# Kernel tuning notes

Measured on AMD Instinct MI355X. Metric: run time of the kernel, lower is better.

## Reference

```python
import jax, jax.numpy as jnp
import numpy as np

N, E = 20000, 160000
F, H, OUT = 256, 8, 128
L = 6            # total layers -> 5 GAT layers
LM1 = L - 1
NGN = L // 3 + 1 # 3 GraphNorms
D = F // H       # 32 per head
GN_FREQ = 3
EPS = 1e-5


def setup_inputs() -> dict:
    key = jax.random.key(0)
    ks = jax.random.split(key, 12)
    x = jax.random.normal(ks[0], (N, 1), dtype=jnp.float32)
    edge_index = jax.random.randint(ks[1], (2, E), 0, N, dtype=jnp.int32)
    W0 = jax.random.normal(ks[2], (1, F), dtype=jnp.float32) * 0.1
    b0 = jnp.zeros((F,), jnp.float32)
    gat_lin = jax.random.normal(ks[3], (LM1, F, F), dtype=jnp.float32) * (1.0 / np.sqrt(F))
    att_src = jax.random.normal(ks[4], (LM1, H, D), dtype=jnp.float32) * 0.1
    att_dst = jax.random.normal(ks[5], (LM1, H, D), dtype=jnp.float32) * 0.1
    gat_bias = jnp.zeros((LM1, F), jnp.float32)
    gn_weight = jnp.ones((NGN, F), jnp.float32)
    gn_bias = jnp.zeros((NGN, F), jnp.float32)
    gn_mean_scale = jnp.ones((NGN, F), jnp.float32)
    lin_W = jax.random.normal(ks[6], (F, OUT), dtype=jnp.float32) * (1.0 / np.sqrt(F))
    lin_b = jnp.zeros((OUT,), jnp.float32)
    return {"x": x, "W0": W0, "b0": b0, "gat_lin": gat_lin, "att_src": att_src,
            "att_dst": att_dst, "gat_bias": gat_bias, "gn_weight": gn_weight,
            "gn_bias": gn_bias, "gn_mean_scale": gn_mean_scale,
            "lin_W": lin_W, "lin_b": lin_b, "edge_index": edge_index}


def _gcn_conv(x, W, b, src, dst, n):
    h = x @ W
    deg = jax.ops.segment_sum(jnp.ones(src.shape[0], h.dtype), dst, num_segments=n)
    dinv = jnp.where(deg > 0, jax.lax.rsqrt(deg), 0.0)
    norm = dinv[src] * dinv[dst]                      # [E']
    out = jax.ops.segment_sum(h[src] * norm[:, None], dst, num_segments=n)
    return out + b


def _gat_conv(x, W, a_src, a_dst, src, dst, n):
    # PyG GATConv (concat=True, negative_slope=0.2, self-loops in src/dst)
    h = (x @ W).reshape(n, H, D)
    s = jnp.einsum('nhd,hd->nh', h, a_src)            # [N,H]
    t = jnp.einsum('nhd,hd->nh', h, a_dst)
    e = jax.nn.leaky_relu(s[src] + t[dst], 0.2)       # [E',H]
    m = jax.ops.segment_max(e, dst, num_segments=n)   # per-dst softmax
    e = jnp.exp(e - m[dst])
    denom = jax.ops.segment_sum(e, dst, num_segments=n)
    alpha = e / (denom[dst] + 1e-16)
    out = jax.ops.segment_sum(h[src] * alpha[:, :, None], dst, num_segments=n)
    return out.reshape(n, F)


def _graph_norm(x, w, b, ms):
    # PyG GraphNorm with batch=None (single graph): per-feature stats over nodes
    mean = jnp.mean(x, axis=0)
    out = x - ms * mean
    var = jnp.mean(out * out, axis=0)
    return w * out * jax.lax.rsqrt(var + EPS) + b


def reference(x, W0, b0, gat_lin, att_src, att_dst, gat_bias, gn_weight, gn_bias,
              gn_mean_scale, lin_W, lin_b, edge_index):
    n = x.shape[0]
    loops = jnp.arange(n, dtype=edge_index.dtype)
    src = jnp.concatenate([edge_index[0], loops])
    dst = jnp.concatenate([edge_index[1], loops])
    h = jax.nn.relu(_gcn_conv(x, W0, b0, src, dst, n))
    for i in range(LM1):
        if i % GN_FREQ == 0:
            g = i // GN_FREQ
            h = _graph_norm(h, gn_weight[g], gn_bias[g], gn_mean_scale[g])
        out = _gat_conv(h, gat_lin[i], att_src[i], att_dst[i], src, dst, n)
        if i % GN_FREQ == 0:
            out = out + gat_bias[i]
        h = h + jax.nn.relu(out)
    return h @ lin_W + lin_b
```

## Files before the change

kernel.cpp:

```cpp
#include <hip/hip_runtime.h>
#include <hip/hip_bf16.h>
#include <stdint.h>

typedef float f32x4 __attribute__((ext_vector_type(4)));
typedef short s16x8 __attribute__((ext_vector_type(8)));

__device__ __forceinline__ float bf2f(unsigned short u) {
    union { unsigned int i; float f; } v; v.i = ((unsigned int)u) << 16; return v.f;
}
__device__ __forceinline__ unsigned short f2bf(float f) {
    union { float f; unsigned int i; } v; v.f = f;
    unsigned int x = v.i;
    return (unsigned short)((x + 0x7fffu + ((x >> 16) & 1u)) >> 16);
}
__device__ __forceinline__ void bfp(unsigned int u, float& lo, float& hi) {
    union { unsigned int i; float f; } a, b;
    a.i = u << 16; b.i = u & 0xffff0000u;
    lo = a.f; hi = b.f;
}
__device__ __forceinline__ void gload16(const void* g, void* l) {
    __builtin_amdgcn_global_load_lds(
        (const __attribute__((address_space(1))) void*)g,
        (__attribute__((address_space(3))) void*)l, 16, 0, 0);
}

__global__ void k_prep(const int* __restrict__ ei, int E, int* __restrict__ deg,
                       int CB,
                       const float* __restrict__ gat_lin,
                       const float* __restrict__ lin_W,
                       const float* __restrict__ att_src,
                       const float* __restrict__ att_dst,
                       unsigned short* __restrict__ Wt,
                       unsigned short* __restrict__ lt) {
    int bid = blockIdx.x;
    if (bid < CB) {
        int e = bid * 256 + threadIdx.x;
        if (e < E) atomicAdd(&deg[ei[E + e]], 1);
        return;
    }
    int idx = (bid - CB) * 256 + threadIdx.x;
    const int T1 = 5 * 65536;
    const int T2 = T1 + 128 * 256;
    const int T3 = T2 + 5 * 64 * 256;
    if (idx < T1) {
        int l = idx >> 16, r = idx & 0xFFFF;
        int nrow = r >> 8, k = r & 255;
        Wt[(size_t)l * 81920 + nrow * 256 + k] =
            f2bf(gat_lin[(size_t)l * 65536 + k * 256 + nrow]);
    } else if (idx < T2) {
        int j = idx - T1;
        int nrow = j >> 8, k = j & 255;
        lt[nrow * 256 + k] = f2bf(lin_W[(size_t)k * 128 + nrow]);
    } else if (idx < T3) {
        int j = idx - T2;
        int l = j >> 14, r = j & 16383;
        int row = r >> 8, k = r & 255;
        float v = 0.f;
        if (row < 16) {
            int head = row & 7;
            const float* a = (row < 8) ? (att_src + l * 256 + head * 32)
                                       : (att_dst + l * 256 + head * 32);
            const float* wr = gat_lin + (size_t)l * 65536 + k * 256 + head * 32;
#pragma unroll
            for (int d = 0; d < 32; ++d) v += wr[d] * a[d];
        }
        Wt[(size_t)l * 81920 + (256 + row) * 256 + k] = f2bf(v);
    }
}

__global__ __launch_bounds__(256) void k_bsum(const int* __restrict__ deg,
                                              int* __restrict__ bsum, int n) {
    __shared__ int buf[256];
    int i = blockIdx.x * 256 + threadIdx.x;
    buf[threadIdx.x] = (i < n) ? deg[i] + 1 : 0;
    __syncthreads();
#pragma unroll
    for (int off = 128; off > 0; off >>= 1) {
        if ((int)threadIdx.x < off) buf[threadIdx.x] += buf[threadIdx.x + off];
        __syncthreads();
    }
    if (threadIdx.x == 0) bsum[blockIdx.x] = buf[0];
}

__global__ __launch_bounds__(256) void k_scanb(const int* __restrict__ bsum,
                                               int* __restrict__ boff, int nb) {
    __shared__ int buf[256];
    int t = threadIdx.x;
    int v = (t < nb) ? bsum[t] : 0;
    buf[t] = v;
    __syncthreads();
    for (int off = 1; off < 256; off <<= 1) {
        int add = (t >= off) ? buf[t - off] : 0;
        __syncthreads();
        buf[t] += add;
        __syncthreads();
    }
    if (t < nb) boff[t] = buf[t] - v;
}

__global__ __launch_bounds__(256) void k_emit(const int* __restrict__ deg,
                                              const int* __restrict__ boff,
                                              int* __restrict__ rowptr,
                                              int* __restrict__ wo,
                                              float* __restrict__ dinv, int n) {
    __shared__ int buf[256];
    int i = blockIdx.x * 256 + threadIdx.x;
    int v = (i < n) ? deg[i] + 1 : 0;
    buf[threadIdx.x] = v;
    __syncthreads();
    for (int off = 1; off < 256; off <<= 1) {
        int add = ((int)threadIdx.x >= off) ? buf[threadIdx.x - off] : 0;
        __syncthreads();
        buf[threadIdx.x] += add;
        __syncthreads();
    }
    if (i < n) {
        int excl = boff[blockIdx.x] + buf[threadIdx.x] - v;
        rowptr[i] = excl;
        wo[i] = excl;
        dinv[i] = rsqrtf((float)v);
        if (i == n - 1) rowptr[n] = excl + v;
    }
}

__global__ void k_fill(const int* __restrict__ ei, int E, int n,
                       int* wo, int* srcs) {
    int e = blockIdx.x * blockDim.x + threadIdx.x;
    int EP = E + n;
    if (e >= EP) return;
    int s_, d_;
    if (e < E) { s_ = ei[e]; d_ = ei[E + e]; }
    else       { s_ = d_ = e - E; }
    int pos = atomicAdd(&wo[d_], 1);
    srcs[pos] = s_;
}

__global__ __launch_bounds__(256) void k_h0f(const float* __restrict__ x,
                                             const float* __restrict__ dinv,
                                             const int* __restrict__ rowptr,
                                             const int* __restrict__ srcs,
                                             const float* __restrict__ W0,
                                             const float* __restrict__ b0,
                                             unsigned short* __restrict__ hbf,
                                             int n, int Mpad) {
    int wave = threadIdx.x >> 6, lane = threadIdx.x & 63;
    int node = blockIdx.x * 4 + wave;
    if (node >= Mpad) return;
    size_t base = (size_t)node * 256 + lane * 4;
    if (node >= n) {
        ushort4 z = {0, 0, 0, 0};
        *reinterpret_cast<ushort4*>(hbf + base) = z;
        return;
    }
    int p0 = rowptr[node], p1 = rowptr[node + 1];
    float sum = 0.f;
    for (int p = p0 + lane; p < p1; p += 64) {
        int s = srcs[p];
        sum += x[s] * dinv[s];
    }
#pragma unroll
    for (int m = 1; m < 64; m <<= 1) sum += __shfl_xor(sum, m);
    float sv = sum * dinv[node];
    float4 wv = *reinterpret_cast<const float4*>(W0 + lane * 4);
    float4 bv = *reinterpret_cast<const float4*>(b0 + lane * 4);
    ushort4 o;
    o.x = f2bf(fmaxf(sv * wv.x + bv.x, 0.f));
    o.y = f2bf(fmaxf(sv * wv.y + bv.y, 0.f));
    o.z = f2bf(fmaxf(sv * wv.z + bv.z, 0.f));
    o.w = f2bf(fmaxf(sv * wv.w + bv.w, 0.f));
    *reinterpret_cast<ushort4*>(hbf + base) = o;
}

__global__ __launch_bounds__(256) void k_gn_reduce(const unsigned short* __restrict__ hbf,
                                                   float* sums, float* sumsq, int n) {
    int f = threadIdx.x;
    float s = 0.f, q = 0.f;
    for (int r = blockIdx.x; r < n; r += gridDim.x) {
        float v = bf2f(hbf[(size_t)r * 256 + f]);
        s += v; q += v * v;
    }
    atomicAdd(&sums[f], s);
    atomicAdd(&sumsq[f], q);
}

__global__ __launch_bounds__(256) void k_gnfold(const float* __restrict__ st,
                                                const float* __restrict__ w,
                                                const float* __restrict__ b,
                                                const float* __restrict__ ms,
                                                unsigned short* __restrict__ Wt,
                                                float* __restrict__ so,
                                                float* __restrict__ rowbias,
                                                float ninv) {
    __shared__ float red[256];
    int col = blockIdx.x, k = threadIdx.x;
    float mean = st[k] * ninv;
    float m2   = st[256 + k] * ninv;
    float msf  = ms[k];
    float var  = m2 + msf * mean * mean * (msf - 2.0f);
    float sc = w[k] * rsqrtf(var + 1e-5f);
    float of = b[k] - msf * mean * sc;
    size_t idx = (size_t)col * 256 + k;
    float wv = bf2f(Wt[idx]);
    red[k] = of * wv;
    __syncthreads();
#pragma unroll
    for (int off = 128; off > 0; off >>= 1) {
        if (k < off) red[k] += red[k + off];
        __syncthreads();
    }
    if (k == 0) rowbias[col] = red[0];
    Wt[idx] = f2bf(sc * wv);
    if (col == 0) { so[k] = sc; so[256 + k] = of; }
}

#define BM 64
__global__ __launch_bounds__(512) void k_gemm_mfma(
    const unsigned short* __restrict__ A,
    const unsigned short* __restrict__ Bt,
    unsigned short* __restrict__ Cb,
    float* __restrict__ Cf,
    float* __restrict__ sbuf,
    float* __restrict__ tbuf,
    const float* __restrict__ bias,
    const float* __restrict__ rowbias,
    int M, int ldc)
{
    __shared__ unsigned short As[64 * 256];
    __shared__ unsigned short Bs[64 * 256];
    const int tid = threadIdx.x;
    const int bm = blockIdx.x * BM;
    const int bn = blockIdx.y * 64;
    {
        const char* ga = (const char*)(A + (size_t)bm * 256);
        const char* gb = (const char*)(Bt + (size_t)bn * 256);
        char* la = (char*)As;
        char* lb = (char*)Bs;
#pragma unroll
        for (int i = 0; i < 4; ++i) {
            int o  = (i * 512 + tid) * 16;
            int so = o ^ (((o >> 9) & 7) << 4);
            gload16(ga + so, la + o);
            gload16(gb + so, lb + o);
        }
    }
    __syncthreads();

    const int lane = tid & 63;
    const int w  = tid >> 6;
    const int wm = (w >> 1) * 16;
    const int wn = (w & 1) * 32;
    const int r  = lane & 15, kb = lane >> 4;
    const int r4 = (lane >> 4) * 4, cc = lane & 15;
    const char* la = (const char*)As;
    const char* lb = (const char*)Bs;

    f32x4 acc[2] = {};
#pragma unroll
    for (int ks = 0; ks < 8; ++ks) {
        int row = wm + r;
        int c16 = (ks * 4 + kb) ^ (row & 7);
        s16x8 af = *(const s16x8*)(la + row * 512 + c16 * 16);
#pragma unroll
        for (int j = 0; j < 2; ++j) {
            int col = wn + j * 16 + r;
            int d16 = (ks * 4 + kb) ^ (col & 7);
            s16x8 bfr = *(const s16x8*)(lb + col * 512 + d16 * 16);
            acc[j] = __builtin_amdgcn_mfma_f32_16x16x32_bf16(af, bfr, acc[j], 0, 0, 0);
        }
    }
#pragma unroll
    for (int j = 0; j < 2; ++j) {
        int col = bn + wn + j * 16 + cc;
        float rb = rowbias ? rowbias[col] : 0.f;
#pragma unroll
        for (int q = 0; q < 4; ++q) {
            int row = bm + wm + r4 + q;
            float v = acc[j][q] + rb;
            if (Cb) {
                if (col < 256) {
                    Cb[(size_t)row * 256 + col] = f2bf(v);
                } else if (col < 264) {
                    sbuf[(size_t)row * 8 + (col - 256)] = v;
                } else if (col < 272) {
                    tbuf[(size_t)row * 8 + (col - 264)] = v;
                }
            } else if (row < M) {
                Cf[(size_t)row * ldc + col] = v + bias[col];
            }
        }
    }
}

__global__ __launch_bounds__(256) void k_fagg(const unsigned short* __restrict__ h1,
                                              const float* __restrict__ sbuf,
                                              const float* __restrict__ tbuf,
                                              const int* __restrict__ rowptr,
                                              const int* __restrict__ srcs,
                                              unsigned short* __restrict__ hbf,
                                              const float* __restrict__ bias,
                                              const float* __restrict__ so, int n) {
    int wave = threadIdx.x >> 6, lane = threadIdx.x & 63;
    int node = blockIdx.x * 4 + wave;
    if (node >= n) return;
    int p0 = rowptr[node], p1 = rowptr[node + 1];
    int hid = lane >> 5;
    int l5 = lane & 31;
    int fl = l5 * 8;
    int head = l5 >> 2;
    float tv = tbuf[node * 8 + head];
    float m = -1e30f, den = 0.f;
    float a0 = 0.f, a1 = 0.f, a2 = 0.f, a3 = 0.f;
    float a4 = 0.f, a5 = 0.f, a6 = 0.f, a7 = 0.f;
    int q = p0 + hid;
    for (; q + 2 < p1; q += 4) {
        int s0 = srcs[q], s1 = srcs[q + 2];
        float e0 = sbuf[s0 * 8 + head] + tv;
        float e1 = sbuf[s1 * 8 + head] + tv;
        uint4 v0 = *reinterpret_cast<const uint4*>(h1 + (size_t)s0 * 256 + fl);
        uint4 v1 = *reinterpret_cast<const uint4*>(h1 + (size_t)s1 * 256 + fl);
        e0 = (e0 > 0.f) ? e0 : 0.2f * e0;
        e1 = (e1 > 0.f) ? e1 : 0.2f * e1;
        float em = fmaxf(e0, e1);
        if (em > m + 8.f) {
            float sc = __expf(m - em);
            den *= sc;
            a0 *= sc; a1 *= sc; a2 *= sc; a3 *= sc;
            a4 *= sc; a5 *= sc; a6 *= sc; a7 *= sc;
            m = em;
        }
        float w0 = __expf(e0 - m), w1 = __expf(e1 - m);
        den += w0 + w1;
        float f0l, f0h, f1l, f1h;
        bfp(v0.x, f0l, f0h); bfp(v1.x, f1l, f1h);
        a0 += w0 * f0l + w1 * f1l;
        a1 += w0 * f0h + w1 * f1h;
        bfp(v0.y, f0l, f0h); bfp(v1.y, f1l, f1h);
        a2 += w0 * f0l + w1 * f1l;
        a3 += w0 * f0h + w1 * f1h;
        bfp(v0.z, f0l, f0h); bfp(v1.z, f1l, f1h);
        a4 += w0 * f0l + w1 * f1l;
        a5 += w0 * f0h + w1 * f1h;
        bfp(v0.w, f0l, f0h); bfp(v1.w, f1l, f1h);
        a6 += w0 * f0l + w1 * f1l;
        a7 += w0 * f0h + w1 * f1h;
    }
    for (; q < p1; q += 2) {
        int s0 = srcs[q];
        float e0 = sbuf[s0 * 8 + head] + tv;
        uint4 v0 = *reinterpret_cast<const uint4*>(h1 + (size_t)s0 * 256 + fl);
        e0 = (e0 > 0.f) ? e0 : 0.2f * e0;
        if (e0 > m + 8.f) {
            float sc = __expf(m - e0);
            den *= sc;
            a0 *= sc; a1 *= sc; a2 *= sc; a3 *= sc;
            a4 *= sc; a5 *= sc; a6 *= sc; a7 *= sc;
            m = e0;
        }
        float w0 = __expf(e0 - m);
        den += w0;
        float f0l, f0h;
        bfp(v0.x, f0l, f0h); a0 += w0 * f0l; a1 += w0 * f0h;
        bfp(v0.y, f0l, f0h); a2 += w0 * f0l; a3 += w0 * f0h;
        bfp(v0.z, f0l, f0h); a4 += w0 * f0l; a5 += w0 * f0h;
        bfp(v0.w, f0l, f0h); a6 += w0 * f0l; a7 += w0 * f0h;
    }
    float mo = __shfl_xor(m, 32);
    float mm = fmaxf(m, mo);
    float sc = __expf(m - mm);
    den *= sc; den += __shfl_xor(den, 32);
    a0 *= sc; a0 += __shfl_xor(a0, 32);
    a1 *= sc; a1 += __shfl_xor(a1, 32);
    a2 *= sc; a2 += __shfl_xor(a2, 32);
    a3 *= sc; a3 += __shfl_xor(a3, 32);
    a4 *= sc; a4 += __shfl_xor(a4, 32);
    a5 *= sc; a5 += __shfl_xor(a5, 32);
    a6 *= sc; a6 += __shfl_xor(a6, 32);
    a7 *= sc; a7 += __shfl_xor(a7, 32);
    if (hid) return;
    float inv = 1.0f / (den + 1e-16f);
    a0 *= inv; a1 *= inv; a2 *= inv; a3 *= inv;
    a4 *= inv; a5 *= inv; a6 *= inv; a7 *= inv;
    float b_[8] = {0.f, 0.f, 0.f, 0.f, 0.f, 0.f, 0.f, 0.f};
    if (bias) {
        float4 blo = *reinterpret_cast<const float4*>(bias + fl);
        float4 bhi = *reinterpret_cast<const float4*>(bias + fl + 4);
        b_[0] = blo.x; b_[1] = blo.y; b_[2] = blo.z; b_[3] = blo.w;
        b_[4] = bhi.x; b_[5] = bhi.y; b_[6] = bhi.z; b_[7] = bhi.w;
    }
    size_t base = (size_t)node * 256 + fl;
    uint4 hv = *reinterpret_cast<const uint4*>(hbf + base);
    float h_[8];
    bfp(hv.x, h_[0], h_[1]); bfp(hv.y, h_[2], h_[3]);
    bfp(hv.z, h_[4], h_[5]); bfp(hv.w, h_[6], h_[7]);
    if (so) {
        float4 s0v = *reinterpret_cast<const float4*>(so + fl);
        float4 s1v = *reinterpret_cast<const float4*>(so + fl + 4);
        float4 o0v = *reinterpret_cast<const float4*>(so + 256 + fl);
        float4 o1v = *reinterpret_cast<const float4*>(so + 256 + fl + 4);
        h_[0] = h_[0] * s0v.x + o0v.x; h_[1] = h_[1] * s0v.y + o0v.y;
        h_[2] = h_[2] * s0v.z + o0v.z; h_[3] = h_[3] * s0v.w + o0v.w;
        h_[4] = h_[4] * s1v.x + o1v.x; h_[5] = h_[5] * s1v.y + o1v.y;
        h_[6] = h_[6] * s1v.z + o1v.z; h_[7] = h_[7] * s1v.w + o1v.w;
    }
    float r0 = h_[0] + fmaxf(a0 + b_[0], 0.f);
    float r1 = h_[1] + fmaxf(a1 + b_[1], 0.f);
    float r2 = h_[2] + fmaxf(a2 + b_[2], 0.f);
    float r3 = h_[3] + fmaxf(a3 + b_[3], 0.f);
    float r4 = h_[4] + fmaxf(a4 + b_[4], 0.f);
    float r5 = h_[5] + fmaxf(a5 + b_[5], 0.f);
    float r6 = h_[6] + fmaxf(a6 + b_[6], 0.f);
    float r7 = h_[7] + fmaxf(a7 + b_[7], 0.f);
    uint4 o;
    o.x = (unsigned int)f2bf(r0) | ((unsigned int)f2bf(r1) << 16);
    o.y = (unsigned int)f2bf(r2) | ((unsigned int)f2bf(r3) << 16);
    o.z = (unsigned int)f2bf(r4) | ((unsigned int)f2bf(r5) << 16);
    o.w = (unsigned int)f2bf(r6) | ((unsigned int)f2bf(r7) << 16);
    *reinterpret_cast<uint4*>(hbf + base) = o;
}

extern "C" void kernel_launch(void* const* d_in, const int* in_sizes, int n_in,
                              void* d_out, int out_size, void* d_ws, size_t ws_size,
                              hipStream_t stream) {
    const float* x        = (const float*)d_in[0];
    const float* W0       = (const float*)d_in[1];
    const float* b0       = (const float*)d_in[2];
    const float* gat_lin  = (const float*)d_in[3];
    const float* att_src  = (const float*)d_in[4];
    const float* att_dst  = (const float*)d_in[5];
    const float* gat_bias = (const float*)d_in[6];
    const float* gn_w     = (const float*)d_in[7];
    const float* gn_b     = (const float*)d_in[8];
    const float* gn_ms    = (const float*)d_in[9];
    const float* lin_W    = (const float*)d_in[10];
    const float* lin_b    = (const float*)d_in[11];
    const int*   ei       = (const int*)d_in[12];

    const int n  = in_sizes[0];
    const int E  = in_sizes[12] / 2;
    const int EP = E + n;
    const int Mpad = ((n + BM - 1) / BM) * BM;
    const int nb = (n + 255) / 256;

    char* w = (char*)d_ws;
    unsigned short* hbf = (unsigned short*)w; w += (size_t)Mpad * 256 * 2;
    unsigned short* h1  = (unsigned short*)w; w += (size_t)Mpad * 256 * 2;
    float* sbuf = (float*)w;                  w += (size_t)Mpad * 8 * 4;
    float* tbuf = (float*)w;                  w += (size_t)Mpad * 8 * 4;
    unsigned short* Wt = (unsigned short*)w;  w += (size_t)5 * 320 * 256 * 2;
    unsigned short* lt = (unsigned short*)w;  w += (size_t)128 * 256 * 2;
    float* scaleoff = (float*)w;              w += 1024 * 4;
    float* rowbias  = (float*)w;              w += 640 * 4;
    float* gnstat = (float*)w;                w += 1024 * 4;
    int* deg    = (int*)w;                    w += (size_t)n * 4;
    float* dinv = (float*)w;                  w += (size_t)n * 4;
    int* rowptr = (int*)w;                    w += ((size_t)(n + 1) * 4 + 15) / 16 * 16;
    int* wo     = (int*)w;                    w += (size_t)n * 4;
    int* bsum   = (int*)w;                    w += ((size_t)nb * 4 + 15) / 16 * 16;
    int* boff   = (int*)w;                    w += ((size_t)nb * 4 + 15) / 16 * 16;
    int* srcs   = (int*)w;                    w += (size_t)EP * 4;

    const int B256 = 256;
    auto cdiv = [](int a, int b) { return (a + b - 1) / b; };

    hipMemsetAsync(gnstat, 0, 1024 * 4 + (size_t)n * 4, stream);

    const int CB = cdiv(E, B256);
    const int WPREP = 5 * 65536 + 128 * 256 + 5 * 64 * 256;
    k_prep<<<CB + cdiv(WPREP, B256), B256, 0, stream>>>(
        ei, E, deg, CB, gat_lin, lin_W, att_src, att_dst, Wt, lt);

    k_bsum<<<nb, 256, 0, stream>>>(deg, bsum, n);
    k_scanb<<<1, 256, 0, stream>>>(bsum, boff, nb);
    k_emit<<<nb, 256, 0, stream>>>(deg, boff, rowptr, wo, dinv, n);
    k_fill<<<cdiv(EP, B256), B256, 0, stream>>>(ei, E, n, wo, srcs);

    k_h0f<<<cdiv(Mpad, 4), 256, 0, stream>>>(x, dinv, rowptr, srcs, W0, b0, hbf, n, Mpad);

    const float ninv = 1.0f / (float)n;
    const int gx = Mpad / BM;

    for (int i = 0; i < 5; ++i) {
        const float* rb = nullptr;
        const float* so = nullptr;
        if (i % 3 == 0) {
            int g = i / 3;
            k_gn_reduce<<<256, 256, 0, stream>>>(hbf, gnstat + g * 512,
                                                 gnstat + g * 512 + 256, n);
            k_gnfold<<<320, 256, 0, stream>>>(gnstat + g * 512, gn_w + g * 256,
                                              gn_b + g * 256, gn_ms + g * 256,
                                              Wt + (size_t)i * 81920,
                                              scaleoff + g * 512, rowbias + g * 320, ninv);
            rb = rowbias + g * 320;
            so = scaleoff + g * 512;
        }
        k_gemm_mfma<<<dim3(gx, 5), 512, 0, stream>>>(
            hbf, Wt + (size_t)i * 81920, h1, nullptr, sbuf, tbuf, nullptr, rb,
            n, 256);
        k_fagg<<<cdiv(n, 4), 256, 0, stream>>>(
            h1, sbuf, tbuf, rowptr, srcs, hbf,
            (i % 3 == 0) ? gat_bias + i * 256 : nullptr, so, n);
    }

    k_gemm_mfma<<<dim3(gx, 2), 512, 0, stream>>>(
        hbf, lt, nullptr, (float*)d_out, nullptr, nullptr, lin_b, nullptr,
        n, 128);
}
```

Baseline: 282.0 us.

## Fuse whole GNN pipeline into one persistent cooperative megakernel

Replaces the chain of about twenty small kernel launches (CSR build, GCN layer, GraphNorm, GEMMs, aggregations) with a single cooperative kernel. Phases are separated by grid-wide syncs, and the GEMM becomes a persistent tile loop. The aim is to remove per-launch overhead and the idle gaps between the many short kernels. In exchange it adds grid-sync costs, runs each phase on a capped grid size, and keeps the multi-kernel path as a fallback.

```diff
diff --git a/kernel.cpp b/kernel.cpp
--- a/kernel.cpp
+++ b/kernel.cpp
@@ -1,6 +1,9 @@
 #include <hip/hip_runtime.h>
+#include <hip/hip_cooperative_groups.h>
 #include <hip/hip_bf16.h>
 #include <stdint.h>
+
+namespace cg = cooperative_groups;
 
 typedef float f32x4 __attribute__((ext_vector_type(4)));
 typedef short s16x8 __attribute__((ext_vector_type(8)));
@@ -24,284 +27,124 @@
         (__attribute__((address_space(3))) void*)l, 16, 0, 0);
 }
 
-__global__ void k_prep(const int* __restrict__ ei, int E, int* __restrict__ deg,
-                       int CB,
-                       const float* __restrict__ gat_lin,
-                       const float* __restrict__ lin_W,
-                       const float* __restrict__ att_src,
-                       const float* __restrict__ att_dst,
-                       unsigned short* __restrict__ Wt,
-                       unsigned short* __restrict__ lt) {
-    int bid = blockIdx.x;
-    if (bid < CB) {
-        int e = bid * 256 + threadIdx.x;
-        if (e < E) atomicAdd(&deg[ei[E + e]], 1);
-        return;
-    }
-    int idx = (bid - CB) * 256 + threadIdx.x;
+struct Params {
+    const float *x, *W0, *b0, *gat_lin, *att_src, *att_dst, *gat_bias;
+    const float *gn_w, *gn_b, *gn_ms, *lin_W, *lin_b;
+    const int* ei;
+    float* out;
+    unsigned short *hbf, *h1, *Wt, *lt;
+    float *sbuf, *tbuf, *scaleoff, *rowbias, *gnstat, *dinv;
+    int *deg, *rowptr, *wo, *bsum, *srcs;
+    int n, E, EP, Mpad, nb;
+};
+
+__device__ __forceinline__ void wconv_body(const Params& P, int idx) {
     const int T1 = 5 * 65536;
     const int T2 = T1 + 128 * 256;
-    const int T3 = T2 + 5 * 64 * 256;
     if (idx < T1) {
         int l = idx >> 16, r = idx & 0xFFFF;
         int nrow = r >> 8, k = r & 255;
-        Wt[(size_t)l * 81920 + nrow * 256 + k] =
-            f2bf(gat_lin[(size_t)l * 65536 + k * 256 + nrow]);
+        P.Wt[(size_t)l * 81920 + nrow * 256 + k] =
+            f2bf(P.gat_lin[(size_t)l * 65536 + k * 256 + nrow]);
     } else if (idx < T2) {
         int j = idx - T1;
         int nrow = j >> 8, k = j & 255;
-        lt[nrow * 256 + k] = f2bf(lin_W[(size_t)k * 128 + nrow]);
-    } else if (idx < T3) {
+        P.lt[nrow * 256 + k] = f2bf(P.lin_W[(size_t)k * 128 + nrow]);
+    } else {
         int j = idx - T2;
         int l = j >> 14, r = j & 16383;
         int row = r >> 8, k = r & 255;
         float v = 0.f;
         if (row < 16) {
             int head = row & 7;
-            const float* a = (row < 8) ? (att_src + l * 256 + head * 32)
-                                       : (att_dst + l * 256 + head * 32);
-            const float* wr = gat_lin + (size_t)l * 65536 + k * 256 + head * 32;
+            const float* a = (row < 8) ? (P.att_src + l * 256 + head * 32)
+                                       : (P.att_dst + l * 256 + head * 32);
+            const float* wr = P.gat_lin + (size_t)l * 65536 + k * 256 + head * 32;
 #pragma unroll
             for (int d = 0; d < 32; ++d) v += wr[d] * a[d];
         }
-        Wt[(size_t)l * 81920 + (256 + row) * 256 + k] = f2bf(v);
-    }
-}
-
-__global__ __launch_bounds__(256) void k_bsum(const int* __restrict__ deg,
-                                              int* __restrict__ bsum, int n) {
-    __shared__ int buf[256];
-    int i = blockIdx.x * 256 + threadIdx.x;
-    buf[threadIdx.x] = (i < n) ? deg[i] + 1 : 0;
-    __syncthreads();
-#pragma unroll
-    for (int off = 128; off > 0; off >>= 1) {
-        if ((int)threadIdx.x < off) buf[threadIdx.x] += buf[threadIdx.x + off];
-        __syncthreads();
-    }
-    if (threadIdx.x == 0) bsum[blockIdx.x] = buf[0];
-}
-
-__global__ __launch_bounds__(256) void k_scanb(const int* __restrict__ bsum,
-                                               int* __restrict__ boff, int nb) {
-    __shared__ int buf[256];
-    int t = threadIdx.x;
-    int v = (t < nb) ? bsum[t] : 0;
-    buf[t] = v;
-    __syncthreads();
-    for (int off = 1; off < 256; off <<= 1) {
-        int add = (t >= off) ? buf[t - off] : 0;
-        __syncthreads();
-        buf[t] += add;
-        __syncthreads();
-    }
-    if (t < nb) boff[t] = buf[t] - v;
-}
-
-__global__ __launch_bounds__(256) void k_emit(const int* __restrict__ deg,
-                                              const int* __restrict__ boff,
-                                              int* __restrict__ rowptr,
-                                              int* __restrict__ wo,
-                                              float* __restrict__ dinv, int n) {
-    __shared__ int buf[256];
-    int i = blockIdx.x * 256 + threadIdx.x;
-    int v = (i < n) ? deg[i] + 1 : 0;
-    buf[threadIdx.x] = v;
-    __syncthreads();
-    for (int off = 1; off < 256; off <<= 1) {
-        int add = ((int)threadIdx.x >= off) ? buf[threadIdx.x - off] : 0;
-        __syncthreads();
-        buf[threadIdx.x] += add;
-        __syncthreads();
-    }
-    if (i < n) {
-        int excl = boff[blockIdx.x] + buf[threadIdx.x] - v;
-        rowptr[i] = excl;
-        wo[i] = excl;
-        dinv[i] = rsqrtf((float)v);
-        if (i == n - 1) rowptr[n] = excl + v;
-    }
-}
-
-__global__ void k_fill(const int* __restrict__ ei, int E, int n,
-                       int* wo, int* srcs) {
-    int e = blockIdx.x * blockDim.x + threadIdx.x;
-    int EP = E + n;
-    if (e >= EP) return;
-    int s_, d_;
-    if (e < E) { s_ = ei[e]; d_ = ei[E + e]; }
-    else       { s_ = d_ = e - E; }
-    int pos = atomicAdd(&wo[d_], 1);
-    srcs[pos] = s_;
-}
-
-__global__ __launch_bounds__(256) void k_h0f(const float* __restrict__ x,
-                                             const float* __restrict__ dinv,
-                                             const int* __restrict__ rowptr,
-                                             const int* __restrict__ srcs,
-                                             const float* __restrict__ W0,
-                                             const float* __restrict__ b0,
-                                             unsigned short* __restrict__ hbf,
-                                             int n, int Mpad) {
-    int wave = threadIdx.x >> 6, lane = threadIdx.x & 63;
-    int node = blockIdx.x * 4 + wave;
-    if (node >= Mpad) return;
-    size_t base = (size_t)node * 256 + lane * 4;
-    if (node >= n) {
-        ushort4 z = {0, 0, 0, 0};
-        *reinterpret_cast<ushort4*>(hbf + base) = z;
-        return;
-    }
-    int p0 = rowptr[node], p1 = rowptr[node + 1];
-    float sum = 0.f;
-    for (int p = p0 + lane; p < p1; p += 64) {
-        int s = srcs[p];
-        sum += x[s] * dinv[s];
-    }
-#pragma unroll
-    for (int m = 1; m < 64; m <<= 1) sum += __shfl_xor(sum, m);
-    float sv = sum * dinv[node];
-    float4 wv = *reinterpret_cast<const float4*>(W0 + lane * 4);
-    float4 bv = *reinterpret_cast<const float4*>(b0 + lane * 4);
-    ushort4 o;
-    o.x = f2bf(fmaxf(sv * wv.x + bv.x, 0.f));
-    o.y = f2bf(fmaxf(sv * wv.y + bv.y, 0.f));
-    o.z = f2bf(fmaxf(sv * wv.z + bv.z, 0.f));
-    o.w = f2bf(fmaxf(sv * wv.w + bv.w, 0.f));
-    *reinterpret_cast<ushort4*>(hbf + base) = o;
-}
-
-__global__ __launch_bounds__(256) void k_gn_reduce(const unsigned short* __restrict__ hbf,
-                                                   float* sums, float* sumsq, int n) {
-    int f = threadIdx.x;
-    float s = 0.f, q = 0.f;
-    for (int r = blockIdx.x; r < n; r += gridDim.x) {
-        float v = bf2f(hbf[(size_t)r * 256 + f]);
-        s += v; q += v * v;
-    }
-    atomicAdd(&sums[f], s);
-    atomicAdd(&sumsq[f], q);
-}
-
-__global__ __launch_bounds__(256) void k_gnfold(const float* __restrict__ st,
-                                                const float* __restrict__ w,
-                                                const float* __restrict__ b,
-                                                const float* __restrict__ ms,
-                                                unsigned short* __restrict__ Wt,
-                                                float* __restrict__ so,
-                                                float* __restrict__ rowbias,
-                                                float ninv) {
-    __shared__ float red[256];
-    int col = blockIdx.x, k = threadIdx.x;
-    float mean = st[k] * ninv;
-    float m2   = st[256 + k] * ninv;
-    float msf  = ms[k];
-    float var  = m2 + msf * mean * mean * (msf - 2.0f);
-    float sc = w[k] * rsqrtf(var + 1e-5f);
-    float of = b[k] - msf * mean * sc;
-    size_t idx = (size_t)col * 256 + k;
-    float wv = bf2f(Wt[idx]);
-    red[k] = of * wv;
-    __syncthreads();
-#pragma unroll
-    for (int off = 128; off > 0; off >>= 1) {
-        if (k < off) red[k] += red[k + off];
-        __syncthreads();
-    }
-    if (k == 0) rowbias[col] = red[0];
-    Wt[idx] = f2bf(sc * wv);
-    if (col == 0) { so[k] = sc; so[256 + k] = of; }
-}
-
-#define BM 64
-__global__ __launch_bounds__(512) void k_gemm_mfma(
-    const unsigned short* __restrict__ A,
-    const unsigned short* __restrict__ Bt,
-    unsigned short* __restrict__ Cb,
-    float* __restrict__ Cf,
-    float* __restrict__ sbuf,
-    float* __restrict__ tbuf,
-    const float* __restrict__ bias,
-    const float* __restrict__ rowbias,
-    int M, int ldc)
+        P.Wt[(size_t)l * 81920 + (256 + row) * 256 + k] = f2bf(v);
+    }
+}
+
+__device__ __forceinline__ void gemm_phase(
+    const unsigned short* A, const unsigned short* Bt,
+    unsigned short* Cb, float* Cf, float* sbuf, float* tbuf,
+    const float* bias, const float* rowbias,
+    int M, int ldc, int npan, int Mpad,
+    unsigned short* As, unsigned short* Bs)
 {
-    __shared__ unsigned short As[64 * 256];
-    __shared__ unsigned short Bs[64 * 256];
     const int tid = threadIdx.x;
-    const int bm = blockIdx.x * BM;
-    const int bn = blockIdx.y * 64;
-    {
-        const char* ga = (const char*)(A + (size_t)bm * 256);
-        const char* gb = (const char*)(Bt + (size_t)bn * 256);
-        char* la = (char*)As;
-        char* lb = (char*)Bs;
-#pragma unroll
-        for (int i = 0; i < 4; ++i) {
-            int o  = (i * 512 + tid) * 16;
-            int so = o ^ (((o >> 9) & 7) << 4);
-            gload16(ga + so, la + o);
-            gload16(gb + so, lb + o);
-        }
-    }
-    __syncthreads();
-
+    const int gx = Mpad >> 6;
+    const int ntiles = gx * npan;
     const int lane = tid & 63;
     const int w  = tid >> 6;
     const int wm = (w >> 1) * 16;
     const int wn = (w & 1) * 32;
     const int r  = lane & 15, kb = lane >> 4;
     const int r4 = (lane >> 4) * 4, cc = lane & 15;
-    const char* la = (const char*)As;
-    const char* lb = (const char*)Bs;
-
-    f32x4 acc[2] = {};
-#pragma unroll
-    for (int ks = 0; ks < 8; ++ks) {
-        int row = wm + r;
-        int c16 = (ks * 4 + kb) ^ (row & 7);
-        s16x8 af = *(const s16x8*)(la + row * 512 + c16 * 16);
+    for (int t = blockIdx.x; t < ntiles; t += gridDim.x) {
+        int bx = t % gx, by = t / gx;
+        int bm = bx * 64, bn = by * 64;
+        __syncthreads();
+        {
+            const char* ga = (const char*)(A + (size_t)bm * 256);
+            const char* gb = (const char*)(Bt + (size_t)bn * 256);
+#pragma unroll
+            for (int i2 = 0; i2 < 4; ++i2) {
+                int o  = (i2 * 512 + tid) * 16;
+                int so = o ^ (((o >> 9) & 7) << 4);
+                gload16(ga + so, (char*)As + o);
+                gload16(gb + so, (char*)Bs + o);
+            }
+        }
+        __syncthreads();
+        f32x4 acc[2] = {};
+#pragma unroll
+        for (int ks = 0; ks < 8; ++ks) {
+            int row = wm + r;
+            int c16 = (ks * 4 + kb) ^ (row & 7);
+            s16x8 af = *(const s16x8*)((char*)As + row * 512 + c16 * 16);
+#pragma unroll
+            for (int j = 0; j < 2; ++j) {
+                int col = wn + j * 16 + r;
+                int d16 = (ks * 4 + kb) ^ (col & 7);
+                s16x8 bfr = *(const s16x8*)((char*)Bs + col * 512 + d16 * 16);
+                acc[j] = __builtin_amdgcn_mfma_f32_16x16x32_bf16(af, bfr, acc[j], 0, 0, 0);
+            }
+        }
 #pragma unroll
         for (int j = 0; j < 2; ++j) {
-            int col = wn + j * 16 + r;
-            int d16 = (ks * 4 + kb) ^ (col & 7);
-            s16x8 bfr = *(const s16x8*)(lb + col * 512 + d16 * 16);
-            acc[j] = __builtin_amdgcn_mfma_f32_16x16x32_bf16(af, bfr, acc[j], 0, 0, 0);
-        }
-    }
-#pragma unroll
-    for (int j = 0; j < 2; ++j) {
-        int col = bn + wn + j * 16 + cc;
-        float rb = rowbias ? rowbias[col] : 0.f;
-#pragma unroll
-        for (int q = 0; q < 4; ++q) {
-            int row = bm + wm + r4 + q;
-            float v = acc[j][q] + rb;
-            if (Cb) {
-                if (col < 256) {
-                    Cb[(size_t)row * 256 + col] = f2bf(v);
-                } else if (col < 264) {
-                    sbuf[(size_t)row * 8 + (col - 256)] = v;
-                } else if (col < 272) {
-                    tbuf[(size_t)row * 8 + (col - 264)] = v;
+            int col = bn + wn + j * 16 + cc;
+            float rbv = rowbias ? rowbias[col] : 0.f;
+#pragma unroll
+            for (int q2 = 0; q2 < 4; ++q2) {
+                int row = bm + wm + r4 + q2;
+                float v = acc[j][q2] + rbv;
+                if (Cb) {
+                    if (col < 256) {
+                        Cb[(size_t)row * 256 + col] = f2bf(v);
+                    } else if (col < 264) {
+                        sbuf[(size_t)row * 8 + (col - 256)] = v;
+                    } else if (col < 272) {
+                        tbuf[(size_t)row * 8 + (col - 264)] = v;
+                    }
+                } else if (row < M) {
+                    Cf[(size_t)row * ldc + col] = v + bias[col];
                 }
-            } else if (row < M) {
-                Cf[(size_t)row * ldc + col] = v + bias[col];
             }
         }
     }
 }
 
-__global__ __launch_bounds__(256) void k_fagg(const unsigned short* __restrict__ h1,
-                                              const float* __restrict__ sbuf,
-                                              const float* __restrict__ tbuf,
-                                              const int* __restrict__ rowptr,
-                                              const int* __restrict__ srcs,
-                                              unsigned short* __restrict__ hbf,
-                                              const float* __restrict__ bias,
-                                              const float* __restrict__ so, int n) {
-    int wave = threadIdx.x >> 6, lane = threadIdx.x & 63;
-    int node = blockIdx.x * 4 + wave;
-    if (node >= n) return;
+__device__ __forceinline__ void fagg_body(
+    const unsigned short* __restrict__ h1,
+    const float* __restrict__ sbuf, const float* __restrict__ tbuf,
+    const int* __restrict__ rowptr, const int* __restrict__ srcs,
+    unsigned short* __restrict__ hbf,
+    const float* __restrict__ bias, const float* __restrict__ so,
+    int node, int lane)
+{
     int p0 = rowptr[node], p1 = rowptr[node + 1];
     int hid = lane >> 5;
     int l5 = lane & 31;
@@ -418,90 +261,439 @@
     *reinterpret_cast<uint4*>(hbf + base) = o;
 }
 
-extern "C" void kernel_launch(void* const* d_in, const int* in_sizes, int n_in,
-                              void* d_out, int out_size, void* d_ws, size_t ws_size,
-                              hipStream_t stream) {
-    const float* x        = (const float*)d_in[0];
-    const float* W0       = (const float*)d_in[1];
-    const float* b0       = (const float*)d_in[2];
-    const float* gat_lin  = (const float*)d_in[3];
-    const float* att_src  = (const float*)d_in[4];
-    const float* att_dst  = (const float*)d_in[5];
-    const float* gat_bias = (const float*)d_in[6];
-    const float* gn_w     = (const float*)d_in[7];
-    const float* gn_b     = (const float*)d_in[8];
-    const float* gn_ms    = (const float*)d_in[9];
-    const float* lin_W    = (const float*)d_in[10];
-    const float* lin_b    = (const float*)d_in[11];
-    const int*   ei       = (const int*)d_in[12];
-
-    const int n  = in_sizes[0];
-    const int E  = in_sizes[12] / 2;
-    const int EP = E + n;
-    const int Mpad = ((n + BM - 1) / BM) * BM;
-    const int nb = (n + 255) / 256;
-
-    char* w = (char*)d_ws;
-    unsigned short* hbf = (unsigned short*)w; w += (size_t)Mpad * 256 * 2;
-    unsigned short* h1  = (unsigned short*)w; w += (size_t)Mpad * 256 * 2;
-    float* sbuf = (float*)w;                  w += (size_t)Mpad * 8 * 4;
-    float* tbuf = (float*)w;                  w += (size_t)Mpad * 8 * 4;
-    unsigned short* Wt = (unsigned short*)w;  w += (size_t)5 * 320 * 256 * 2;
-    unsigned short* lt = (unsigned short*)w;  w += (size_t)128 * 256 * 2;
-    float* scaleoff = (float*)w;              w += 1024 * 4;
-    float* rowbias  = (float*)w;              w += 640 * 4;
-    float* gnstat = (float*)w;                w += 1024 * 4;
-    int* deg    = (int*)w;                    w += (size_t)n * 4;
-    float* dinv = (float*)w;                  w += (size_t)n * 4;
-    int* rowptr = (int*)w;                    w += ((size_t)(n + 1) * 4 + 15) / 16 * 16;
-    int* wo     = (int*)w;                    w += (size_t)n * 4;
-    int* bsum   = (int*)w;                    w += ((size_t)nb * 4 + 15) / 16 * 16;
-    int* boff   = (int*)w;                    w += ((size_t)nb * 4 + 15) / 16 * 16;
-    int* srcs   = (int*)w;                    w += (size_t)EP * 4;
-
-    const int B256 = 256;
-    auto cdiv = [](int a, int b) { return (a + b - 1) / b; };
-
-    hipMemsetAsync(gnstat, 0, 1024 * 4 + (size_t)n * 4, stream);
-
-    const int CB = cdiv(E, B256);
-    const int WPREP = 5 * 65536 + 128 * 256 + 5 * 64 * 256;
-    k_prep<<<CB + cdiv(WPREP, B256), B256, 0, stream>>>(
-        ei, E, deg, CB, gat_lin, lin_W, att_src, att_dst, Wt, lt);
-
-    k_bsum<<<nb, 256, 0, stream>>>(deg, bsum, n);
-    k_scanb<<<1, 256, 0, stream>>>(bsum, boff, nb);
-    k_emit<<<nb, 256, 0, stream>>>(deg, boff, rowptr, wo, dinv, n);
-    k_fill<<<cdiv(EP, B256), B256, 0, stream>>>(ei, E, n, wo, srcs);
-
-    k_h0f<<<cdiv(Mpad, 4), 256, 0, stream>>>(x, dinv, rowptr, srcs, W0, b0, hbf, n, Mpad);
-
-    const float ninv = 1.0f / (float)n;
-    const int gx = Mpad / BM;
-
+__device__ __forceinline__ void h0_body(const Params& P, int node, int lane) {
+    size_t base = (size_t)node * 256 + lane * 4;
+    if (node >= P.n) {
+        ushort4 z = {0, 0, 0, 0};
+        *reinterpret_cast<ushort4*>(P.hbf + base) = z;
+        return;
+    }
+    int p0 = P.rowptr[node], p1 = P.rowptr[node + 1];
+    float sum = 0.f;
+    for (int p = p0 + lane; p < p1; p += 64) {
+        int s = P.srcs[p];
+        sum += P.x[s] * P.dinv[s];
+    }
+#pragma unroll
+    for (int m = 1; m < 64; m <<= 1) sum += __shfl_xor(sum, m);
+    float sv = sum * P.dinv[node];
+    float4 wv = *reinterpret_cast<const float4*>(P.W0 + lane * 4);
+    float4 bv = *reinterpret_cast<const float4*>(P.b0 + lane * 4);
+    ushort4 o;
+    o.x = f2bf(fmaxf(sv * wv.x + bv.x, 0.f));
+    o.y = f2bf(fmaxf(sv * wv.y + bv.y, 0.f));
+    o.z = f2bf(fmaxf(sv * wv.z + bv.z, 0.f));
+    o.w = f2bf(fmaxf(sv * wv.w + bv.w, 0.f));
+    *reinterpret_cast<ushort4*>(P.hbf + base) = o;
+}
+
+__global__ __launch_bounds__(512, 4) void k_mega(Params P) {
+    __shared__ unsigned short As[64 * 256];
+    __shared__ unsigned short Bs[64 * 256];
+    cg::grid_group grid = cg::this_grid();
+    const int tid  = threadIdx.x;
+    const int bid  = blockIdx.x;
+    const int nblk = gridDim.x;
+    const int gtid = bid * 512 + tid;
+    const int nthr = nblk * 512;
+    const int lane = tid & 63;
+    const int wid  = tid >> 6;
+    const int gw   = bid * 8 + wid;
+    const int nw   = nblk * 8;
+
+    for (int i = gtid; i < P.n; i += nthr) P.deg[i] = 0;
+    for (int i = gtid; i < 1024; i += nthr) P.gnstat[i] = 0.f;
+    {
+        const int T3 = 5 * 65536 + 128 * 256 + 5 * 64 * 256;
+        for (int idx = gtid; idx < T3; idx += nthr) wconv_body(P, idx);
+    }
+    grid.sync();
+    for (int e = gtid; e < P.E; e += nthr) atomicAdd(&P.deg[P.ei[P.E + e]], 1);
+    grid.sync();
+    for (int c = gw; c < P.nb; c += nw) {
+        int base = c * 256;
+        int s = 0;
+#pragma unroll
+        for (int j = 0; j < 4; ++j) {
+            int i = base + j * 64 + lane;
+            s += (i < P.n) ? P.deg[i] + 1 : 0;
+        }
+#pragma unroll
+        for (int m = 1; m < 64; m <<= 1) s += __shfl_xor(s, m);
+        if (lane == 0) P.bsum[c] = s;
+    }
+    grid.sync();
+    for (int c = gw; c < P.nb; c += nw) {
+        int off = 0;
+        for (int j = lane; j < c; j += 64) off += P.bsum[j];
+#pragma unroll
+        for (int m = 1; m < 64; m <<= 1) off += __shfl_xor(off, m);
+        int base = c * 256 + lane * 4;
+        int v[4];
+#pragma unroll
+        for (int j = 0; j < 4; ++j) {
+            int i = base + j;
+            v[j] = (i < P.n) ? P.deg[i] + 1 : 0;
+        }
+        int vsum = v[0] + v[1] + v[2] + v[3];
+        int incl = vsum;
+        for (int d = 1; d < 64; d <<= 1) {
+            int t = __shfl_up(incl, d);
+            if (lane >= d) incl += t;
+        }
+        int run = off + incl - vsum;
+#pragma unroll
+        for (int j = 0; j < 4; ++j) {
+            int i = base + j;
+            if (i < P.n) {
+                P.rowptr[i] = run;
+                P.wo[i] = run;
+                P.dinv[i] = rsqrtf((float)v[j]);
+                run += v[j];
+                if (i == P.n - 1) P.rowptr[P.n] = run;
+            }
+        }
+    }
+    grid.sync();
+    for (int e = gtid; e < P.EP; e += nthr) {
+        int s_, d_;
+        if (e < P.E) { s_ = P.ei[e]; d_ = P.ei[P.E + e]; }
+        else         { s_ = d_ = e - P.E; }
+        int pos = atomicAdd(&P.wo[d_], 1);
+        P.srcs[pos] = s_;
+    }
+    grid.sync();
+    for (int node = gw; node < P.Mpad; node += nw) h0_body(P, node, lane);
+    grid.sync();
     for (int i = 0; i < 5; ++i) {
         const float* rb = nullptr;
         const float* so = nullptr;
         if (i % 3 == 0) {
             int g = i / 3;
-            k_gn_reduce<<<256, 256, 0, stream>>>(hbf, gnstat + g * 512,
-                                                 gnstat + g * 512 + 256, n);
-            k_gnfold<<<320, 256, 0, stream>>>(gnstat + g * 512, gn_w + g * 256,
-                                              gn_b + g * 256, gn_ms + g * 256,
-                                              Wt + (size_t)i * 81920,
-                                              scaleoff + g * 512, rowbias + g * 320, ninv);
-            rb = rowbias + g * 320;
-            so = scaleoff + g * 512;
-        }
-        k_gemm_mfma<<<dim3(gx, 5), 512, 0, stream>>>(
-            hbf, Wt + (size_t)i * 81920, h1, nullptr, sbuf, tbuf, nullptr, rb,
-            n, 256);
-        k_fagg<<<cdiv(n, 4), 256, 0, stream>>>(
-            h1, sbuf, tbuf, rowptr, srcs, hbf,
-            (i % 3 == 0) ? gat_bias + i * 256 : nullptr, so, n);
-    }
-
-    k_gemm_mfma<<<dim3(gx, 2), 512, 0, stream>>>(
-        hbf, lt, nullptr, (float*)d_out, nullptr, nullptr, lin_b, nullptr,
-        n, 128);
-}
+            float* st = P.gnstat + g * 512;
+            {
+                int f = tid & 255, half = tid >> 8;
+                float s = 0.f, q = 0.f;
+                for (int r = bid * 2 + half; r < P.n; r += nblk * 2) {
+                    float v = bf2f(P.hbf[(size_t)r * 256 + f]);
+                    s += v; q += v * v;
+                }
+                atomicAdd(&st[f], s);
+                atomicAdd(&st[256 + f], q);
+            }
+            grid.sync();
+            {
+                unsigned short* Wl = P.Wt + (size_t)i * 81920;
+                float ninv = 1.f / (float)P.n;
+                for (int col = gw; col < 320; col += nw) {
+                    float partial = 0.f;
+#pragma unroll
+                    for (int j = 0; j < 4; ++j) {
+                        int k = lane * 4 + j;
+                        float mean = st[k] * ninv;
+                        float m2   = st[256 + k] * ninv;
+                        float msf  = P.gn_ms[g * 256 + k];
+                        float var  = m2 + msf * mean * mean * (msf - 2.0f);
+                        float sc = P.gn_w[g * 256 + k] * rsqrtf(var + 1e-5f);
+                        float of = P.gn_b[g * 256 + k] - msf * mean * sc;
+                        size_t idx = (size_t)col * 256 + k;
+                        float wv = bf2f(Wl[idx]);
+                        partial += of * wv;
+                        Wl[idx] = f2bf(sc * wv);
+                        if (col == 0) {
+                            P.scaleoff[g * 512 + k] = sc;
+                            P.scaleoff[g * 512 + 256 + k] = of;
+                        }
+                    }
+#pragma unroll
+                    for (int m = 1; m < 64; m <<= 1) partial += __shfl_xor(partial, m);
+                    if (lane == 0) P.rowbias[g * 320 + col] = partial;
+                }
+            }
+            grid.sync();
+            rb = P.rowbias + g * 320;
+            so = P.scaleoff + g * 512;
+        }
+        gemm_phase(P.hbf, P.Wt + (size_t)i * 81920, P.h1, nullptr,
+                   P.sbuf, P.tbuf, nullptr, rb, P.n, 256, 5, P.Mpad, As, Bs);
+        grid.sync();
+        {
+            const float* bias = (i % 3 == 0) ? P.gat_bias + i * 256 : nullptr;
+            for (int node = gw; node < P.n; node += nw)
+                fagg_body(P.h1, P.sbuf, P.tbuf, P.rowptr, P.srcs, P.hbf,
+                          bias, so, node, lane);
+        }
+        grid.sync();
+    }
+    gemm_phase(P.hbf, P.lt, nullptr, P.out, nullptr, nullptr,
+               P.lin_b, nullptr, P.n, 128, 2, P.Mpad, As, Bs);
+}
+
+__global__ void k_prep(Params P, int CB) {
+    int bid = blockIdx.x;
+    if (bid < CB) {
+        int e = bid * 256 + threadIdx.x;
+        if (e < P.E) atomicAdd(&P.deg[P.ei[P.E + e]], 1);
+        return;
+    }
+    int idx = (bid - CB) * 256 + threadIdx.x;
+    const int T3 = 5 * 65536 + 128 * 256 + 5 * 64 * 256;
+    if (idx < T3) wconv_body(P, idx);
+}
+
+__global__ __launch_bounds__(256) void k_bsum(Params P) {
+    __shared__ int buf[256];
+    int i = blockIdx.x * 256 + threadIdx.x;
+    buf[threadIdx.x] = (i < P.n) ? P.deg[i] + 1 : 0;
+    __syncthreads();
+#pragma unroll
+    for (int off = 128; off > 0; off >>= 1) {
+        if ((int)threadIdx.x < off) buf[threadIdx.x] += buf[threadIdx.x + off];
+        __syncthreads();
+    }
+    if (threadIdx.x == 0) P.bsum[blockIdx.x] = buf[0];
+}
+
+__global__ __launch_bounds__(256) void k_emit(Params P) {
+    __shared__ int buf[256];
+    int t = threadIdx.x;
+    int bid = blockIdx.x;
+    buf[t] = (t < bid) ? P.bsum[t] : 0;
+    __syncthreads();
+#pragma unroll
+    for (int off = 128; off > 0; off >>= 1) {
+        if (t < off) buf[t] += buf[t + off];
+        __syncthreads();
+    }
+    int boff = buf[0];
+    __syncthreads();
+    int i = bid * 256 + t;
+    int v = (i < P.n) ? P.deg[i] + 1 : 0;
+    buf[t] = v;
+    __syncthreads();
+    for (int off = 1; off < 256; off <<= 1) {
+        int add = (t >= off) ? buf[t - off] : 0;
+        __syncthreads();
+        buf[t] += add;
+        __syncthreads();
+    }
+    if (i < P.n) {
+        int excl = boff + buf[t] - v;
+        P.rowptr[i] = excl;
+        P.wo[i] = excl;
+        P.dinv[i] = rsqrtf((float)v);
+        if (i == P.n - 1) P.rowptr[P.n] = excl + v;
+    }
+}
+
+__global__ void k_fill(Params P) {
+    int e = blockIdx.x * blockDim.x + threadIdx.x;
+    if (e >= P.EP) return;
+    int s_, d_;
+    if (e < P.E) { s_ = P.ei[e]; d_ = P.ei[P.E + e]; }
+    else         { s_ = d_ = e - P.E; }
+    int pos = atomicAdd(&P.wo[d_], 1);
+    P.srcs[pos] = s_;
+}
+
+__global__ __launch_bounds__(256) void k_h0f(Params P) {
+    int wave = threadIdx.x >> 6, lane = threadIdx.x & 63;
+    int node = blockIdx.x * 4 + wave;
+    if (node >= P.Mpad) return;
+    h0_body(P, node, lane);
+}
+
+__global__ __launch_bounds__(256) void k_gn_reduce(Params P, int g) {
+    int f = threadIdx.x;
+    float s = 0.f, q = 0.f;
+    for (int r = blockIdx.x; r < P.n; r += gridDim.x) {
+        float v = bf2f(P.hbf[(size_t)r * 256 + f]);
+        s += v; q += v * v;
+    }
+    atomicAdd(&P.gnstat[g * 512 + f], s);
+    atomicAdd(&P.gnstat[g * 512 + 256 + f], q);
+}
+
+__global__ __launch_bounds__(256) void k_gnfold(Params P, int i) {
+    __shared__ float red[256];
+    int g = i / 3;
+    const float* st = P.gnstat + g * 512;
+    int col = blockIdx.x, k = threadIdx.x;
+    float ninv = 1.f / (float)P.n;
+    float mean = st[k] * ninv;
+    float m2   = st[256 + k] * ninv;
+    float msf  = P.gn_ms[g * 256 + k];
+    float var  = m2 + msf * mean * mean * (msf - 2.0f);
+    float sc = P.gn_w[g * 256 + k] * rsqrtf(var + 1e-5f);
+    float of = P.gn_b[g * 256 + k] - msf * mean * sc;
+    unsigned short* Wl = P.Wt + (size_t)i * 81920;
+    size_t idx = (size_t)col * 256 + k;
+    float wv = bf2f(Wl[idx]);
+    red[k] = of * wv;
+    __syncthreads();
+#pragma unroll
+    for (int off = 128; off > 0; off >>= 1) {
+        if (k < off) red[k] += red[k + off];
+        __syncthreads();
+    }
+    if (k == 0) P.rowbias[g * 320 + col] = red[0];
+    Wl[idx] = f2bf(sc * wv);
+    if (col == 0) { P.scaleoff[g * 512 + k] = sc; P.scaleoff[g * 512 + 256 + k] = of; }
+}
+
+__global__ __launch_bounds__(512) void k_gemm(Params P, const unsigned short* Bt,
+                                              unsigned short* Cb, float* Cf,
+                                              const float* bias, const float* rowbias,
+                                              int ldc, int npan) {
+    __shared__ unsigned short As[64 * 256];
+    __shared__ unsigned short Bs[64 * 256];
+    const int tid = threadIdx.x;
+    const int gx = P.Mpad >> 6;
+    int t = blockIdx.x;
+    int bx = t % gx, by = t / gx;
+    int bm = bx * 64, bn = by * 64;
+    {
+        const char* ga = (const char*)(P.hbf + (size_t)bm * 256);
+        const char* gb = (const char*)(Bt + (size_t)bn * 256);
+#pragma unroll
+        for (int i2 = 0; i2 < 4; ++i2) {
+            int o  = (i2 * 512 + tid) * 16;
+            int so = o ^ (((o >> 9) & 7) << 4);
+            gload16(ga + so, (char*)As + o);
+            gload16(gb + so, (char*)Bs + o);
+        }
+    }
+    __syncthreads();
+    const int lane = tid & 63;
+    const int w  = tid >> 6;
+    const int wm = (w >> 1) * 16;
+    const int wn = (w & 1) * 32;
+    const int r  = lane & 15, kb = lane >> 4;
+    const int r4 = (lane >> 4) * 4, cc = lane & 15;
+    f32x4 acc[2] = {};
+#pragma unroll
+    for (int ks = 0; ks < 8; ++ks) {
+        int row = wm + r;
+        int c16 = (ks * 4 + kb) ^ (row & 7);
+        s16x8 af = *(const s16x8*)((char*)As + row * 512 + c16 * 16);
+#pragma unroll
+        for (int j = 0; j < 2; ++j) {
+            int col = wn + j * 16 + r;
+            int d16 = (ks * 4 + kb) ^ (col & 7);
+            s16x8 bfr = *(const s16x8*)((char*)Bs + col * 512 + d16 * 16);
+            acc[j] = __builtin_amdgcn_mfma_f32_16x16x32_bf16(af, bfr, acc[j], 0, 0, 0);
+        }
+    }
+#pragma unroll
+    for (int j = 0; j < 2; ++j) {
+        int col = bn + wn + j * 16 + cc;
+        float rbv = rowbias ? rowbias[col] : 0.f;
+#pragma unroll
+        for (int q2 = 0; q2 < 4; ++q2) {
+            int row = bm + wm + r4 + q2;
+            float v = acc[j][q2] + rbv;
+            if (Cb) {
+                if (col < 256) {
+                    Cb[(size_t)row * 256 + col] = f2bf(v);
+                } else if (col < 264) {
+                    P.sbuf[(size_t)row * 8 + (col - 256)] = v;
+                } else if (col < 272) {
+                    P.tbuf[(size_t)row * 8 + (col - 264)] = v;
+                }
+            } else if (row < P.n) {
+                Cf[(size_t)row * ldc + col] = v + bias[col];
+            }
+        }
+    }
+}
+
+__global__ __launch_bounds__(256) void k_fagg(Params P, const float* bias,
+                                              const float* so) {
+    int wave = threadIdx.x >> 6, lane = threadIdx.x & 63;
+    int node = blockIdx.x * 4 + wave;
+    if (node >= P.n) return;
+    fagg_body(P.h1, P.sbuf, P.tbuf, P.rowptr, P.srcs, P.hbf, bias, so, node, lane);
+}
+
+extern "C" void kernel_launch(void* const* d_in, const int* in_sizes, int n_in,
+                              void* d_out, int out_size, void* d_ws, size_t ws_size,
+                              hipStream_t stream) {
+    Params P;
+    P.x        = (const float*)d_in[0];
+    P.W0       = (const float*)d_in[1];
+    P.b0       = (const float*)d_in[2];
+    P.gat_lin  = (const float*)d_in[3];
+    P.att_src  = (const float*)d_in[4];
+    P.att_dst  = (const float*)d_in[5];
+    P.gat_bias = (const float*)d_in[6];
+    P.gn_w     = (const float*)d_in[7];
+    P.gn_b     = (const float*)d_in[8];
+    P.gn_ms    = (const float*)d_in[9];
+    P.lin_W    = (const float*)d_in[10];
+    P.lin_b    = (const float*)d_in[11];
+    P.ei       = (const int*)d_in[12];
+    P.out      = (float*)d_out;
+
+    P.n  = in_sizes[0];
+    P.E  = in_sizes[12] / 2;
+    P.EP = P.E + P.n;
+    P.Mpad = ((P.n + 63) / 64) * 64;
+    P.nb = (P.n + 255) / 256;
+
+    char* w = (char*)d_ws;
+    P.hbf = (unsigned short*)w;      w += (size_t)P.Mpad * 256 * 2;
+    P.h1  = (unsigned short*)w;      w += (size_t)P.Mpad * 256 * 2;
+    P.sbuf = (float*)w;              w += (size_t)P.Mpad * 8 * 4;
+    P.tbuf = (float*)w;              w += (size_t)P.Mpad * 8 * 4;
+    P.Wt = (unsigned short*)w;       w += (size_t)5 * 320 * 256 * 2;
+    P.lt = (unsigned short*)w;       w += (size_t)128 * 256 * 2;
+    P.scaleoff = (float*)w;          w += 1024 * 4;
+    P.rowbias  = (float*)w;          w += 640 * 4;
+    P.gnstat = (float*)w;            w += 1024 * 4;
+    P.deg    = (int*)w;              w += (size_t)P.n * 4;
+    P.dinv   = (float*)w;            w += (size_t)P.n * 4;
+    P.rowptr = (int*)w;              w += ((size_t)(P.n + 1) * 4 + 15) / 16 * 16;
+    P.wo     = (int*)w;              w += (size_t)P.n * 4;
+    P.bsum   = (int*)w;              w += ((size_t)P.nb * 4 + 15) / 16 * 16;
+    P.srcs   = (int*)w;              w += (size_t)P.EP * 4;
+
+    int occ = 0;
+    hipError_t qerr = hipOccupancyMaxActiveBlocksPerMultiprocessor(&occ, k_mega, 512, 0);
+    bool mega_ok = (qerr == hipSuccess && occ >= 1);
+    if (mega_ok) {
+        int gridBlocks = occ * 256;
+        if (gridBlocks > 1024) gridBlocks = 1024;
+        void* args[] = { &P };
+        hipError_t lerr = hipLaunchCooperativeKernel(
+            (const void*)k_mega, dim3(gridBlocks), dim3(512), args, 0, stream);
+        if (lerr == hipSuccess) return;
+    }
+
+    auto cdiv = [](int a, int b) { return (a + b - 1) / b; };
+    hipMemsetAsync(P.gnstat, 0, 1024 * 4 + (size_t)P.n * 4, stream);
+    const int CB = cdiv(P.E, 256);
+    const int WPREP = 5 * 65536 + 128 * 256 + 5 * 64 * 256;
+    k_prep<<<CB + cdiv(WPREP, 256), 256, 0, stream>>>(P, CB);
+    k_bsum<<<P.nb, 256, 0, stream>>>(P);
+    k_emit<<<P.nb, 256, 0, stream>>>(P);
+    k_fill<<<cdiv(P.EP, 256), 256, 0, stream>>>(P);
+    k_h0f<<<cdiv(P.Mpad, 4), 256, 0, stream>>>(P);
+    const int gx = P.Mpad / 64;
+    for (int i = 0; i < 5; ++i) {
+        const float* rb = nullptr;
+        const float* so = nullptr;
+        if (i % 3 == 0) {
+            int g = i / 3;
+            k_gn_reduce<<<256, 256, 0, stream>>>(P, g);
+            k_gnfold<<<320, 256, 0, stream>>>(P, i);
+            rb = P.rowbias + g * 320;
+            so = P.scaleoff + g * 512;
+        }
+        k_gemm<<<gx * 5, 512, 0, stream>>>(P, P.Wt + (size_t)i * 81920,
+                                           P.h1, nullptr, nullptr, rb, 256, 5);
+        k_fagg<<<cdiv(P.n, 4), 256, 0, stream>>>(
+            P, (i % 3 == 0) ? P.gat_bias + i * 256 : nullptr, so);
+    }
+    k_gemm<<<gx * 2, 512, 0, stream>>>(P, P.lt, nullptr, P.out, P.lin_b,
+                                       nullptr, 128, 2);
+}
```

Measured after the change: 944.0 us. 3.35x slower.
